# Optimization experiments

Hardware: AMD Instinct MI355X
Metric: run time of the kernel (lower is better)

## Reference

```python
import jax, jax.numpy as jnp
import numpy as np

B, T, C, H = 4, 1024, 1024, 16
HS = C // H  # head_size = 64
EPS = 1e-5


def layer_norm(x, w, b):
    mu = jnp.mean(x, axis=-1, keepdims=True)
    var = jnp.mean(jnp.square(x - mu), axis=-1, keepdims=True)
    return (x - mu) * jax.lax.rsqrt(var + EPS) * w + b


def setup_inputs() -> dict:
    key = jax.random.key(0)
    ks = jax.random.split(key, 12)
    s = 0.02
    return {
        "x": jax.random.normal(ks[0], (B, T, C), jnp.float32),
        "ln1_w": jnp.ones((C,), jnp.float32),
        "ln1_b": jnp.zeros((C,), jnp.float32),
        "Wk": jax.random.normal(ks[1], (H, C, HS), jnp.float32) * s,
        "Wq": jax.random.normal(ks[2], (H, C, HS), jnp.float32) * s,
        "Wv": jax.random.normal(ks[3], (H, C, HS), jnp.float32) * s,
        "Wo": jax.random.normal(ks[4], (C, C), jnp.float32) * s,
        "bo": jnp.zeros((C,), jnp.float32),
        "ln2_w": jnp.ones((C,), jnp.float32),
        "ln2_b": jnp.zeros((C,), jnp.float32),
        "W1": jax.random.normal(ks[5], (C, 4 * C), jnp.float32) * s,
        "b1": jnp.zeros((4 * C,), jnp.float32),
        "prelu_a": jnp.asarray(0.25, jnp.float32),
        "W2": jax.random.normal(ks[6], (4 * C, C), jnp.float32) * s,
        "b2": jnp.zeros((C,), jnp.float32),
    }


def reference(x, ln1_w, ln1_b, Wk, Wq, Wv, Wo, bo, ln2_w, ln2_b, W1, b1, prelu_a, W2, b2):
    # --- self-attention branch (pre-LN) ---
    h = layer_norm(x, ln1_w, ln1_b)  # [B,T,C]
    k = jnp.einsum('btc,hcd->bhtd', h, Wk)
    q = jnp.einsum('btc,hcd->bhtd', h, Wq)
    v = jnp.einsum('btc,hcd->bhtd', h, Wv)
    # NOTE: source computes k @ q^T (not q @ k^T) scaled by n_embd**-0.5
    wei = jnp.einsum('bhtd,bhsd->bhts', k, q) * (C ** -0.5)  # [B,H,T,T]
    causal = jnp.tril(jnp.ones((T, T), bool))
    wei = jnp.where(causal, wei, -jnp.inf)
    wei = jax.nn.softmax(wei, axis=-1)
    out = jnp.einsum('bhts,bhsd->bthd', wei, v).reshape(B, T, C)
    out = out @ Wo + bo
    x = x + out
    # --- feed-forward branch (pre-LN) ---
    h2 = layer_norm(x, ln2_w, ln2_b)
    f = h2 @ W1 + b1
    f = jnp.where(f > 0, f, prelu_a * f)  # PReLU, single scalar param
    f = f @ W2 + b2
    return x + f
```

## Files before the change

### kernel.cpp

```cpp
#include <hip/hip_runtime.h>


typedef __bf16 bf16_t;
typedef __attribute__((ext_vector_type(8))) __bf16 bfx8;
typedef __attribute__((ext_vector_type(4))) __bf16 bfx4;
typedef __attribute__((ext_vector_type(4))) float f32x4;
typedef __attribute__((ext_vector_type(8))) unsigned short u16x8;
typedef unsigned int u32;

#define MFMA_BF16(a, b, c) __builtin_amdgcn_mfma_f32_16x16x32_bf16((a), (b), (c), 0, 0, 0)
#define GLOAD_LDS16(g, l)                                                     \
  __builtin_amdgcn_global_load_lds((__attribute__((address_space(1))) void*)(g), \
                                   (__attribute__((address_space(3))) void*)(l), 16, 0, 0)

__global__ __launch_bounds__(256) void ln_kernel(const float* __restrict__ x,
                                                 const float* __restrict__ w,
                                                 const float* __restrict__ b,
                                                 bf16_t* __restrict__ out) {
  const int row = blockIdx.x;
  const int tid = threadIdx.x;
  const float4 v = reinterpret_cast<const float4*>(x + (size_t)row * 1024)[tid];
  float s = v.x + v.y + v.z + v.w;
  float s2 = v.x * v.x + v.y * v.y + v.z * v.z + v.w * v.w;
#pragma unroll
  for (int off = 1; off < 64; off <<= 1) {
    s += __shfl_xor(s, off);
    s2 += __shfl_xor(s2, off);
  }
  __shared__ float red[8];
  const int wv = tid >> 6;
  if ((tid & 63) == 0) {
    red[wv] = s;
    red[4 + wv] = s2;
  }
  __syncthreads();
  s = red[0] + red[1] + red[2] + red[3];
  s2 = red[4] + red[5] + red[6] + red[7];
  const float mu = s * (1.0f / 1024.0f);
  const float rs = rsqrtf(s2 * (1.0f / 1024.0f) - mu * mu + 1e-5f);
  const float4 wv4 = reinterpret_cast<const float4*>(w)[tid];
  const float4 bv4 = reinterpret_cast<const float4*>(b)[tid];
  bfx4 o;
  o[0] = (bf16_t)((v.x - mu) * rs * wv4.x + bv4.x);
  o[1] = (bf16_t)((v.y - mu) * rs * wv4.y + bv4.y);
  o[2] = (bf16_t)((v.z - mu) * rs * wv4.z + bv4.z);
  o[3] = (bf16_t)((v.w - mu) * rs * wv4.w + bv4.w);
  reinterpret_cast<bfx4*>(out + (size_t)row * 1024)[tid] = o;
}

__device__ __forceinline__ void tc_body(const float* __restrict__ in,
                                        bf16_t* __restrict__ out, int K, int N, int k0,
                                        int n0, float (*tile)[65], int t) {
  const int rl = t >> 4, cl = (t & 15) * 4;
#pragma unroll
  for (int p = 0; p < 4; ++p) {
    const int r = p * 16 + rl;
    const float4 v = *reinterpret_cast<const float4*>(in + (size_t)(k0 + r) * N + n0 + cl);
    tile[r][cl] = v.x;
    tile[r][cl + 1] = v.y;
    tile[r][cl + 2] = v.z;
    tile[r][cl + 3] = v.w;
  }
  __syncthreads();
#pragma unroll
  for (int p = 0; p < 2; ++p) {
    const int idx = p * 256 + t;
    const int n = idx >> 3, kc = (idx & 7) * 8;
    bfx8 o;
#pragma unroll
    for (int i = 0; i < 8; ++i) o[i] = (bf16_t)tile[kc + i][n];
    *reinterpret_cast<bfx8*>(out + (size_t)(n0 + n) * K + k0 + kc) = o;
  }
}

__global__ __launch_bounds__(256) void transpose_cast(const float* __restrict__ in,
                                                      bf16_t* __restrict__ out, int K,
                                                      int N) {
  __shared__ float tile[64][65];
  tc_body(in, out, K, N, blockIdx.x * 64, blockIdx.y * 64, tile, threadIdx.x);
}

__global__ __launch_bounds__(256) void transpose_qkv(const float* __restrict__ Wq,
                                                     const float* __restrict__ Wk,
                                                     const float* __restrict__ Wv,
                                                     bf16_t* __restrict__ out) {
  __shared__ float tile[64][65];
  const int z = blockIdx.y;
  const int sel = z >> 4, h = z & 15;
  const float* in = ((sel == 0) ? Wq : (sel == 1) ? Wk : Wv) + h * 65536;
  bf16_t* o = out + (size_t)sel * 1048576 + h * 65536;
  tc_body(in, o, 1024, 64, blockIdx.x * 64, 0, tile, threadIdx.x);
}

enum { EPI_QKV = 0, EPI_WO = 1, EPI_MLP1 = 2, EPI_FINAL = 3 };

template <int MF>
__device__ __forceinline__ void stage_tile(const bf16_t* __restrict__ A,
                                           const bf16_t* __restrict__ BT, int K, int row0,
                                           int col0, int k0, bf16_t* sA, bf16_t* sB,
                                           int tid) {
#pragma unroll
  for (int j = 0; j < MF; ++j) {
    const int chunk = j * 256 + tid;
    const int r = chunk >> 3, c = chunk & 7;
    const int cs = c ^ (r & 7);
    GLOAD_LDS16(A + (size_t)(row0 + r) * K + k0 + cs * 8, sA + chunk * 8);
  }
#pragma unroll
  for (int j = 0; j < 4; ++j) {
    const int chunk = j * 256 + tid;
    const int r = chunk >> 3, c = chunk & 7;
    const int cs = c ^ (r & 7);
    GLOAD_LDS16(BT + (size_t)(col0 + r) * K + k0 + cs * 8, sB + chunk * 8);
  }
}

template <int EPI, int BM>
__global__ __launch_bounds__(256) void gemm_bt(
    const bf16_t* __restrict__ A, const bf16_t* __restrict__ BT,
    const float* __restrict__ bias, const float* __restrict__ res,
    const float* __restrict__ prelu, float* __restrict__ outf,
    bf16_t* __restrict__ ob0, bf16_t* __restrict__ ob1, bf16_t* __restrict__ ob2,
    int K, int N) {
  constexpr int MF = BM / 32;
  __shared__ __align__(16) bf16_t sA[2][BM * 64];
  __shared__ __align__(16) bf16_t sB[2][128 * 64];
  const int tid = threadIdx.x;
  const int lane = tid & 63;
  const int w = tid >> 6;
  const int wr = w >> 1, wc = w & 1;
  const int row0 = blockIdx.x * BM, col0 = blockIdx.y * 128;

  f32x4 acc[MF][4] = {};

  stage_tile<MF>(A, BT, K, row0, col0, 0, sA[0], sB[0], tid);
  __syncthreads();

  const int nk = K >> 6;
  for (int t = 0; t < nk; ++t) {
    const int cur = t & 1;
    if (t + 1 < nk)
      stage_tile<MF>(A, BT, K, row0, col0, (t + 1) * 64, sA[cur ^ 1], sB[cur ^ 1], tid);
    const bf16_t* __restrict__ pA = sA[cur];
    const bf16_t* __restrict__ pB = sB[cur];
#pragma unroll
    for (int kk = 0; kk < 2; ++kk) {
      bfx8 af[MF], bfr[4];
#pragma unroll
      for (int m = 0; m < MF; ++m) {
        const int r = wr * (BM / 2) + m * 16 + (lane & 15);
        const int c = (kk * 4 + (lane >> 4)) ^ (r & 7);
        af[m] = *reinterpret_cast<const bfx8*>(pA + r * 64 + c * 8);
      }
#pragma unroll
      for (int n = 0; n < 4; ++n) {
        const int r = wc * 64 + n * 16 + (lane & 15);
        const int c = (kk * 4 + (lane >> 4)) ^ (r & 7);
        bfr[n] = *reinterpret_cast<const bfx8*>(pB + r * 64 + c * 8);
      }
#pragma unroll
      for (int m = 0; m < MF; ++m)
#pragma unroll
        for (int n = 0; n < 4; ++n) acc[m][n] = MFMA_BF16(af[m], bfr[n], acc[m][n]);
    }
    __syncthreads();
  }

  const float pa = (EPI == EPI_MLP1) ? prelu[0] : 0.0f;
#pragma unroll
  for (int m = 0; m < MF; ++m) {
#pragma unroll
    for (int n = 0; n < 4; ++n) {
#pragma unroll
      for (int j = 0; j < 4; ++j) {
        const int row = row0 + wr * (BM / 2) + m * 16 + ((lane >> 4) << 2) + j;
        const int col = col0 + wc * 64 + n * 16 + (lane & 15);
        const float v = acc[m][n][j];
        if (EPI == EPI_QKV) {
          const int sel = col >> 10;
          const int h = (col >> 6) & 15, d = col & 63;
          const int bb = row >> 10, t = row & 1023;
          bf16_t* dst = (sel == 0) ? ob0 : (sel == 1) ? ob1 : ob2;
          dst[((size_t)(bb * 16 + h) * 1024 + t) * 64 + d] = (bf16_t)v;
        } else if (EPI == EPI_MLP1) {
          float t = v + bias[col];
          t = (t > 0.0f) ? t : pa * t;
          ob0[(size_t)row * N + col] = (bf16_t)t;
        } else {
          outf[(size_t)row * N + col] = v + bias[col] + res[(size_t)row * N + col];
        }
      }
    }
  }
}

__global__ __launch_bounds__(256) void attn_kernel(const bf16_t* __restrict__ kproj,
                                                   const bf16_t* __restrict__ qproj,
                                                   const bf16_t* __restrict__ vproj,
                                                   bf16_t* __restrict__ att) {
  __shared__ __align__(16) bf16_t sK[2][64 * 64];
  __shared__ __align__(16) bf16_t sVt[2][64 * 64];
  __shared__ __align__(16) bf16_t sP[4][16 * 64];
  const int tid = threadIdx.x, lane = tid & 63, w = tid >> 6;
  const int g = lane >> 4, l15 = lane & 15;
  const int bh = blockIdx.y;
  const size_t head = (size_t)bh * (1024 * 64);
  const int b = bh >> 4, h = bh & 15;
  const int vrow = 2 * (tid >> 3);
  const int vdb = tid & 7;

  for (int half = 0; half < 2; ++half) {
    const int tb = half ? (15 - (int)blockIdx.x) : (int)blockIdx.x;
    const int t0 = tb * 64;
    const int nsb = tb + 1;

    __syncthreads();

    bfx8 aq0, aq1;
    {
      const bf16_t* qrow = kproj + head + (size_t)(t0 + w * 16 + l15) * 64 + g * 8;
      aq0 = *reinterpret_cast<const bfx8*>(qrow);
      aq1 = *reinterpret_cast<const bfx8*>(qrow + 32);
    }

    {
#pragma unroll
      for (int j = 0; j < 2; ++j) {
        const int chunk = j * 256 + tid;
        const int r = chunk >> 3, c = chunk & 7;
        const int cs = c ^ (r & 7);
        GLOAD_LDS16(qproj + head + (size_t)r * 64 + cs * 8, sK[0] + chunk * 8);
      }
      const bf16_t* vp = vproj + head + (size_t)vrow * 64 + vdb * 8;
      const u16x8 v0 = *reinterpret_cast<const u16x8*>(vp);
      const u16x8 v1 = *reinterpret_cast<const u16x8*>(vp + 64);
#pragma unroll
      for (int i = 0; i < 8; ++i) {
        const int d = vdb * 8 + i;
        const int cc = ((vrow >> 3) ^ i ^ vdb) & 7;
        const u32 pk = ((u32)v1[i] << 16) | (u32)v0[i];
        *reinterpret_cast<u32*>(sVt[0] + d * 64 + cc * 8 + (vrow & 7)) = pk;
      }
    }
    __syncthreads();

    f32x4 accO[4] = {};
    float mrun[4], lrun[4];
#pragma unroll
    for (int j = 0; j < 4; ++j) {
      mrun[j] = -1e30f;
      lrun[j] = 0.0f;
    }

    for (int sb = 0; sb < nsb; ++sb) {
      const int cur = sb & 1;
      const bool pf = (sb + 1 < nsb);
      u16x8 v0n, v1n;
      if (pf) {
        const int s0n = (sb + 1) * 64;
#pragma unroll
        for (int j = 0; j < 2; ++j) {
          const int chunk = j * 256 + tid;
          const int r = chunk >> 3, c = chunk & 7;
          const int cs = c ^ (r & 7);
          GLOAD_LDS16(qproj + head + (size_t)(s0n + r) * 64 + cs * 8, sK[cur ^ 1] + chunk * 8);
        }
        const bf16_t* vp = vproj + head + (size_t)(s0n + vrow) * 64 + vdb * 8;
        v0n = *reinterpret_cast<const u16x8*>(vp);
        v1n = *reinterpret_cast<const u16x8*>(vp + 64);
      }

      f32x4 accS[4] = {};
      const bf16_t* sKc = sK[cur];
#pragma unroll
      for (int kk = 0; kk < 2; ++kk) {
        const bfx8 aq = kk ? aq1 : aq0;
#pragma unroll
        for (int n = 0; n < 4; ++n) {
          const int r = n * 16 + l15;
          const int c = (kk * 4 + g) ^ (r & 7);
          const bfx8 bk = *reinterpret_cast<const bfx8*>(sKc + r * 64 + c * 8);
          accS[n] = MFMA_BF16(aq, bk, accS[n]);
        }
      }

      const int rbase = t0 + w * 16 + (g << 2);
      const int cbase = sb * 64 + l15;
#pragma unroll
      for (int j = 0; j < 4; ++j) {
        const int t = rbase + j;
        float mx = -1e30f;
#pragma unroll
        for (int n = 0; n < 4; ++n) {
          float v = accS[n][j] * 0.03125f;
          v = ((cbase + n * 16) <= t) ? v : -1e30f;
          accS[n][j] = v;
          mx = fmaxf(mx, v);
        }
        mx = fmaxf(mx, __shfl_xor(mx, 1));
        mx = fmaxf(mx, __shfl_xor(mx, 2));
        mx = fmaxf(mx, __shfl_xor(mx, 4));
        mx = fmaxf(mx, __shfl_xor(mx, 8));
        const float mnew = fmaxf(mrun[j], mx);
        const float al = __expf(mrun[j] - mnew);
        float rsum = 0.0f;
#pragma unroll
        for (int n = 0; n < 4; ++n) {
          const float p = __expf(accS[n][j] - mnew);
          accS[n][j] = p;
          rsum += p;
        }
        rsum += __shfl_xor(rsum, 1);
        rsum += __shfl_xor(rsum, 2);
        rsum += __shfl_xor(rsum, 4);
        rsum += __shfl_xor(rsum, 8);
        lrun[j] = lrun[j] * al + rsum;
        mrun[j] = mnew;
#pragma unroll
        for (int n = 0; n < 4; ++n) accO[n][j] *= al;
      }

      bf16_t* sPw = sP[w];
#pragma unroll
      for (int n = 0; n < 4; ++n)
#pragma unroll
        for (int j = 0; j < 4; ++j) {
          const int r = (g << 2) + j;
          const int s = n * 16 + l15;
          const int cc = (s >> 3) ^ (r & 7);
          sPw[r * 64 + cc * 8 + (s & 7)] = (bf16_t)accS[n][j];
        }

      const bf16_t* sVc = sVt[cur];
#pragma unroll
      for (int kk = 0; kk < 2; ++kk) {
        bfx8 ap;
        {
          const int r = l15;
          const int c = (kk * 4 + g) ^ (r & 7);
          ap = *reinterpret_cast<const bfx8*>(sPw + r * 64 + c * 8);
        }
#pragma unroll
        for (int n = 0; n < 4; ++n) {
          const int d = n * 16 + l15;
          const int c = (kk * 4 + g) ^ (d & 7) ^ ((d >> 3) & 7);
          const bfx8 bv = *reinterpret_cast<const bfx8*>(sVc + d * 64 + c * 8);
          accO[n] = MFMA_BF16(ap, bv, accO[n]);
        }
      }

      if (pf) {
#pragma unroll
        for (int i = 0; i < 8; ++i) {
          const int d = vdb * 8 + i;
          const int cc = ((vrow >> 3) ^ i ^ vdb) & 7;
          const u32 pk = ((u32)v1n[i] << 16) | (u32)v0n[i];
          *reinterpret_cast<u32*>(sVt[cur ^ 1] + d * 64 + cc * 8 + (vrow & 7)) = pk;
        }
      }
      __syncthreads();
    }

#pragma unroll
    for (int j = 0; j < 4; ++j) {
      const float inv = 1.0f / lrun[j];
      const int t = t0 + w * 16 + (g << 2) + j;
#pragma unroll
      for (int n = 0; n < 4; ++n) {
        const int d = n * 16 + l15;
        att[((size_t)(b * 1024 + t)) * 1024 + h * 64 + d] = (bf16_t)(accO[n][j] * inv);
      }
    }
  }
}

extern "C" void kernel_launch(void* const* d_in, const int* in_sizes, int n_in,
                              void* d_out, int out_size, void* d_ws, size_t ws_size,
                              hipStream_t stream) {
  (void)in_sizes; (void)n_in; (void)out_size; (void)ws_size;
  const float* x = (const float*)d_in[0];
  const float* ln1w = (const float*)d_in[1];
  const float* ln1b = (const float*)d_in[2];
  const float* Wk = (const float*)d_in[3];
  const float* Wq = (const float*)d_in[4];
  const float* Wv = (const float*)d_in[5];
  const float* Wo = (const float*)d_in[6];
  const float* bo = (const float*)d_in[7];
  const float* ln2w = (const float*)d_in[8];
  const float* ln2b = (const float*)d_in[9];
  const float* W1 = (const float*)d_in[10];
  const float* b1 = (const float*)d_in[11];
  const float* pa = (const float*)d_in[12];
  const float* W2 = (const float*)d_in[13];
  const float* b2 = (const float*)d_in[14];
  float* out = (float*)d_out;
  char* ws = (char*)d_ws;
  const size_t MB = 1ull << 20;
  bf16_t* h1 = (bf16_t*)(ws + 0 * MB);
  bf16_t* h2 = (bf16_t*)(ws + 8 * MB);
  bf16_t* qb = (bf16_t*)(ws + 16 * MB);
  bf16_t* kb = (bf16_t*)(ws + 24 * MB);
  bf16_t* vb = (bf16_t*)(ws + 32 * MB);
  bf16_t* attb = (bf16_t*)(ws + 40 * MB);
  bf16_t* fbuf = (bf16_t*)(ws + 48 * MB);
  bf16_t* WqkvT = (bf16_t*)(ws + 80 * MB);
  bf16_t* WoT = (bf16_t*)(ws + 86 * MB);
  bf16_t* W1T = (bf16_t*)(ws + 88 * MB);
  bf16_t* W2T = (bf16_t*)(ws + 96 * MB);

  transpose_qkv<<<dim3(16, 48), 256, 0, stream>>>(Wq, Wk, Wv, WqkvT);
  transpose_cast<<<dim3(16, 16), 256, 0, stream>>>(Wo, WoT, 1024, 1024);
  transpose_cast<<<dim3(16, 64), 256, 0, stream>>>(W1, W1T, 1024, 4096);
  transpose_cast<<<dim3(64, 16), 256, 0, stream>>>(W2, W2T, 4096, 1024);

  ln_kernel<<<4096, 256, 0, stream>>>(x, ln1w, ln1b, h1);
  gemm_bt<EPI_QKV, 128><<<dim3(32, 24), 256, 0, stream>>>(h1, WqkvT, nullptr, nullptr,
                                                          nullptr, nullptr, qb, kb, vb,
                                                          1024, 3072);
  attn_kernel<<<dim3(8, 64), 256, 0, stream>>>(kb, qb, vb, attb);
  gemm_bt<EPI_WO, 64><<<dim3(64, 8), 256, 0, stream>>>(attb, WoT, bo, x, nullptr, out,
                                                       nullptr, nullptr, nullptr, 1024, 1024);
  ln_kernel<<<4096, 256, 0, stream>>>(out, ln2w, ln2b, h2);
  gemm_bt<EPI_MLP1, 128><<<dim3(32, 32), 256, 0, stream>>>(h2, W1T, b1, nullptr, pa, nullptr,
                                                           fbuf, nullptr, nullptr, 1024, 4096);
  gemm_bt<EPI_FINAL, 64><<<dim3(64, 8), 256, 0, stream>>>(fbuf, W2T, b2, out, nullptr, out,
                                                          nullptr, nullptr, nullptr, 4096, 1024);
}
```

Measured before the change: 227.1 us.

## Load GEMM A operand directly to registers and triple-buffer B tiles in LDS

Restructures the bf16 GEMM so each wave loads its A rows straight from global memory into registers (double-buffered) instead of staging them through shared memory. Only B is staged into LDS, now triple-buffered with a prefetch distance of two, and explicit vmcnt waits plus raw barriers replace the full __syncthreads. The Wo and final-projection GEMMs move from 64-row to 128-row tiles, which halves their grid. The aim is to cut LDS traffic and synchronisation stalls and to overlap loads with MFMA work. The cost is higher register pressure, uncoalesced-ish A loads, fewer blocks for the N=1024 GEMMs, and fragile hand-counted vmcnt values.

```diff
diff --git a/kernel.cpp b/kernel.cpp
--- a/kernel.cpp
+++ b/kernel.cpp
@@ -94,87 +94,110 @@
 
 enum { EPI_QKV = 0, EPI_WO = 1, EPI_MLP1 = 2, EPI_FINAL = 3 };
 
-template <int MF>
-__device__ __forceinline__ void stage_tile(const bf16_t* __restrict__ A,
-                                           const bf16_t* __restrict__ BT, int K, int row0,
-                                           int col0, int k0, bf16_t* sA, bf16_t* sB,
-                                           int tid) {
-#pragma unroll
-  for (int j = 0; j < MF; ++j) {
-    const int chunk = j * 256 + tid;
-    const int r = chunk >> 3, c = chunk & 7;
-    const int cs = c ^ (r & 7);
-    GLOAD_LDS16(A + (size_t)(row0 + r) * K + k0 + cs * 8, sA + chunk * 8);
-  }
+__device__ __forceinline__ void load_a(const bf16_t* __restrict__ A, int K, int rowbase,
+                                       int k0, int l15, int g, bfx8 (&ar)[8]) {
+#pragma unroll
+  for (int m = 0; m < 4; ++m)
+#pragma unroll
+    for (int kk = 0; kk < 2; ++kk)
+      ar[m * 2 + kk] = *reinterpret_cast<const bfx8*>(
+          A + (size_t)(rowbase + m * 16 + l15) * K + k0 + kk * 32 + g * 8);
+}
+
+__device__ __forceinline__ void stage_b(const bf16_t* __restrict__ BT, int K, int col0,
+                                        int k0, bf16_t* sBb, int tid) {
 #pragma unroll
   for (int j = 0; j < 4; ++j) {
     const int chunk = j * 256 + tid;
     const int r = chunk >> 3, c = chunk & 7;
     const int cs = c ^ (r & 7);
-    GLOAD_LDS16(BT + (size_t)(col0 + r) * K + k0 + cs * 8, sB + chunk * 8);
-  }
-}
-
-template <int EPI, int BM>
+    GLOAD_LDS16(BT + (size_t)(col0 + r) * K + k0 + cs * 8, sBb + chunk * 8);
+  }
+}
+
+__device__ __forceinline__ void compute_step(const bf16_t* __restrict__ sBc,
+                                             const bfx8 (&ar)[8], f32x4 (&acc)[4][4],
+                                             int wc, int l15, int g) {
+#pragma unroll
+  for (int kk = 0; kk < 2; ++kk) {
+    bfx8 bfr[4];
+#pragma unroll
+    for (int n = 0; n < 4; ++n) {
+      const int r = wc * 64 + n * 16 + l15;
+      const int c = (kk * 4 + g) ^ (r & 7);
+      bfr[n] = *reinterpret_cast<const bfx8*>(sBc + r * 64 + c * 8);
+    }
+#pragma unroll
+    for (int m = 0; m < 4; ++m)
+#pragma unroll
+      for (int n = 0; n < 4; ++n)
+        acc[m][n] = MFMA_BF16(ar[m * 2 + kk], bfr[n], acc[m][n]);
+  }
+}
+
+template <int EPI>
 __global__ __launch_bounds__(256) void gemm_bt(
     const bf16_t* __restrict__ A, const bf16_t* __restrict__ BT,
     const float* __restrict__ bias, const float* __restrict__ res,
     const float* __restrict__ prelu, float* __restrict__ outf,
     bf16_t* __restrict__ ob0, bf16_t* __restrict__ ob1, bf16_t* __restrict__ ob2,
     int K, int N) {
-  constexpr int MF = BM / 32;
-  __shared__ __align__(16) bf16_t sA[2][BM * 64];
-  __shared__ __align__(16) bf16_t sB[2][128 * 64];
+  __shared__ __align__(16) bf16_t sB[3][128 * 64];
   const int tid = threadIdx.x;
   const int lane = tid & 63;
   const int w = tid >> 6;
   const int wr = w >> 1, wc = w & 1;
-  const int row0 = blockIdx.x * BM, col0 = blockIdx.y * 128;
-
-  f32x4 acc[MF][4] = {};
-
-  stage_tile<MF>(A, BT, K, row0, col0, 0, sA[0], sB[0], tid);
-  __syncthreads();
-
+  const int g = lane >> 4, l15 = lane & 15;
+  const int row0 = blockIdx.x * 128, col0 = blockIdx.y * 128;
+  const int rowbase = row0 + wr * 64;
+
+  f32x4 acc[4][4] = {};
+  bfx8 a0[8], a1[8];
   const int nk = K >> 6;
-  for (int t = 0; t < nk; ++t) {
-    const int cur = t & 1;
-    if (t + 1 < nk)
-      stage_tile<MF>(A, BT, K, row0, col0, (t + 1) * 64, sA[cur ^ 1], sB[cur ^ 1], tid);
-    const bf16_t* __restrict__ pA = sA[cur];
-    const bf16_t* __restrict__ pB = sB[cur];
-#pragma unroll
-    for (int kk = 0; kk < 2; ++kk) {
-      bfx8 af[MF], bfr[4];
-#pragma unroll
-      for (int m = 0; m < MF; ++m) {
-        const int r = wr * (BM / 2) + m * 16 + (lane & 15);
-        const int c = (kk * 4 + (lane >> 4)) ^ (r & 7);
-        af[m] = *reinterpret_cast<const bfx8*>(pA + r * 64 + c * 8);
-      }
-#pragma unroll
-      for (int n = 0; n < 4; ++n) {
-        const int r = wc * 64 + n * 16 + (lane & 15);
-        const int c = (kk * 4 + (lane >> 4)) ^ (r & 7);
-        bfr[n] = *reinterpret_cast<const bfx8*>(pB + r * 64 + c * 8);
-      }
-#pragma unroll
-      for (int m = 0; m < MF; ++m)
-#pragma unroll
-        for (int n = 0; n < 4; ++n) acc[m][n] = MFMA_BF16(af[m], bfr[n], acc[m][n]);
-    }
-    __syncthreads();
+
+  load_a(A, K, rowbase, 0, l15, g, a0);
+  stage_b(BT, K, col0, 0, sB[0], tid);
+  stage_b(BT, K, col0, 64, sB[1], tid);
+
+  __builtin_amdgcn_sched_barrier(0);
+  asm volatile("s_waitcnt vmcnt(4)");
+  __builtin_amdgcn_s_barrier();
+  __builtin_amdgcn_sched_barrier(0);
+  load_a(A, K, rowbase, 64, l15, g, a1);
+  stage_b(BT, K, col0, 128, sB[2], tid);
+  compute_step(sB[0], a0, acc, wc, l15, g);
+
+  int cur = 1;
+  for (int t = 1; t < nk; ++t) {
+    __builtin_amdgcn_sched_barrier(0);
+    if (t == nk - 1)
+      asm volatile("s_waitcnt vmcnt(8)");
+    else
+      asm volatile("s_waitcnt vmcnt(12)");
+    __builtin_amdgcn_s_barrier();
+    __builtin_amdgcn_sched_barrier(0);
+    const int prv = (cur == 0) ? 2 : cur - 1;
+    if (t & 1) {
+      if (t + 1 < nk) load_a(A, K, rowbase, (t + 1) * 64, l15, g, a0);
+      if (t + 2 < nk) stage_b(BT, K, col0, (t + 2) * 64, sB[prv], tid);
+      compute_step(sB[cur], a1, acc, wc, l15, g);
+    } else {
+      if (t + 1 < nk) load_a(A, K, rowbase, (t + 1) * 64, l15, g, a1);
+      if (t + 2 < nk) stage_b(BT, K, col0, (t + 2) * 64, sB[prv], tid);
+      compute_step(sB[cur], a0, acc, wc, l15, g);
+    }
+    cur = (cur == 2) ? 0 : cur + 1;
   }
 
   const float pa = (EPI == EPI_MLP1) ? prelu[0] : 0.0f;
 #pragma unroll
-  for (int m = 0; m < MF; ++m) {
+  for (int m = 0; m < 4; ++m) {
 #pragma unroll
     for (int n = 0; n < 4; ++n) {
 #pragma unroll
       for (int j = 0; j < 4; ++j) {
-        const int row = row0 + wr * (BM / 2) + m * 16 + ((lane >> 4) << 2) + j;
-        const int col = col0 + wc * 64 + n * 16 + (lane & 15);
+        const int row = rowbase + m * 16 + (g << 2) + j;
+        const int col = col0 + wc * 64 + n * 16 + l15;
         const float v = acc[m][n][j];
         if (EPI == EPI_QKV) {
           const int sel = col >> 10;
@@ -414,15 +437,14 @@
   transpose_cast<<<dim3(64, 16), 256, 0, stream>>>(W2, W2T, 4096, 1024);
 
   ln_kernel<<<4096, 256, 0, stream>>>(x, ln1w, ln1b, h1);
-  gemm_bt<EPI_QKV, 128><<<dim3(32, 24), 256, 0, stream>>>(h1, WqkvT, nullptr, nullptr,
-                                                          nullptr, nullptr, qb, kb, vb,
-                                                          1024, 3072);
+  gemm_bt<EPI_QKV><<<dim3(32, 24), 256, 0, stream>>>(h1, WqkvT, nullptr, nullptr, nullptr,
+                                                     nullptr, qb, kb, vb, 1024, 3072);
   attn_kernel<<<dim3(8, 64), 256, 0, stream>>>(kb, qb, vb, attb);
-  gemm_bt<EPI_WO, 64><<<dim3(64, 8), 256, 0, stream>>>(attb, WoT, bo, x, nullptr, out,
-                                                       nullptr, nullptr, nullptr, 1024, 1024);
+  gemm_bt<EPI_WO><<<dim3(32, 8), 256, 0, stream>>>(attb, WoT, bo, x, nullptr, out, nullptr,
+                                                   nullptr, nullptr, 1024, 1024);
   ln_kernel<<<4096, 256, 0, stream>>>(out, ln2w, ln2b, h2);
-  gemm_bt<EPI_MLP1, 128><<<dim3(32, 32), 256, 0, stream>>>(h2, W1T, b1, nullptr, pa, nullptr,
-                                                           fbuf, nullptr, nullptr, 1024, 4096);
-  gemm_bt<EPI_FINAL, 64><<<dim3(64, 8), 256, 0, stream>>>(fbuf, W2T, b2, out, nullptr, out,
-                                                          nullptr, nullptr, nullptr, 4096, 1024);
-}
+  gemm_bt<EPI_MLP1><<<dim3(32, 32), 256, 0, stream>>>(h2, W1T, b1, nullptr, pa, nullptr,
+                                                      fbuf, nullptr, nullptr, 1024, 4096);
+  gemm_bt<EPI_FINAL><<<dim3(32, 8), 256, 0, stream>>>(fbuf, W2T, b2, out, nullptr, out,
+                                                      nullptr, nullptr, nullptr, 4096, 1024);
+}
```

Measured after the change: 364.0 us. +60.3%, slower.

## Generalize GEMM tiling with larger tiles and counted vmcnt pipelining

Applied to the files above, without the earlier changes.

Parameterizes the bf16 GEMM over block tile sizes and thread counts, moving the QKV and MLP1 GEMMs to 256x256 tiles with 512 threads and the Wo/W2 GEMMs to 128x128 tiles. The main loop replaces full __syncthreads with a counted s_waitcnt vmcnt so the next tile's async global-to-LDS loads stay in flight while the current tile computes. The larger tiles raise operand reuse per LDS byte but cut the block count (e.g. 192 or 256 blocks), which risks leaving CUs idle and raising register and LDS pressure.

```diff
diff --git a/kernel.cpp b/kernel.cpp
--- a/kernel.cpp
+++ b/kernel.cpp
@@ -94,87 +94,99 @@
 
 enum { EPI_QKV = 0, EPI_WO = 1, EPI_MLP1 = 2, EPI_FINAL = 3 };
 
-template <int MF>
-__device__ __forceinline__ void stage_tile(const bf16_t* __restrict__ A,
-                                           const bf16_t* __restrict__ BT, int K, int row0,
-                                           int col0, int k0, bf16_t* sA, bf16_t* sB,
-                                           int tid) {
-#pragma unroll
-  for (int j = 0; j < MF; ++j) {
-    const int chunk = j * 256 + tid;
-    const int r = chunk >> 3, c = chunk & 7;
-    const int cs = c ^ (r & 7);
-    GLOAD_LDS16(A + (size_t)(row0 + r) * K + k0 + cs * 8, sA + chunk * 8);
-  }
-#pragma unroll
-  for (int j = 0; j < 4; ++j) {
-    const int chunk = j * 256 + tid;
-    const int r = chunk >> 3, c = chunk & 7;
-    const int cs = c ^ (r & 7);
-    GLOAD_LDS16(BT + (size_t)(col0 + r) * K + k0 + cs * 8, sB + chunk * 8);
-  }
-}
-
-template <int EPI, int BM>
-__global__ __launch_bounds__(256) void gemm_bt(
+template <int EPI, int BM, int BN, int NT>
+__global__ __launch_bounds__(NT, 2) void gemm_bt(
     const bf16_t* __restrict__ A, const bf16_t* __restrict__ BT,
     const float* __restrict__ bias, const float* __restrict__ res,
     const float* __restrict__ prelu, float* __restrict__ outf,
     bf16_t* __restrict__ ob0, bf16_t* __restrict__ ob1, bf16_t* __restrict__ ob2,
     int K, int N) {
-  constexpr int MF = BM / 32;
+  constexpr int WM = 2;
+  constexpr int WN = NT / 64 / WM;
+  constexpr int MF = BM / WM / 16;
+  constexpr int NF = BN / WN / 16;
+  constexpr int ACH = BM * 64 / (NT * 8);
+  constexpr int BCH = BN * 64 / (NT * 8);
+  static_assert(ACH + BCH == 8, "counted vmcnt assumes 8 loads per stage");
   __shared__ __align__(16) bf16_t sA[2][BM * 64];
-  __shared__ __align__(16) bf16_t sB[2][128 * 64];
+  __shared__ __align__(16) bf16_t sB[2][BN * 64];
   const int tid = threadIdx.x;
   const int lane = tid & 63;
   const int w = tid >> 6;
-  const int wr = w >> 1, wc = w & 1;
-  const int row0 = blockIdx.x * BM, col0 = blockIdx.y * 128;
-
-  f32x4 acc[MF][4] = {};
-
-  stage_tile<MF>(A, BT, K, row0, col0, 0, sA[0], sB[0], tid);
-  __syncthreads();
-
+  const int wr = w / WN, wc = w % WN;
+  const int g = lane >> 4, l15 = lane & 15;
+  const int row0 = blockIdx.x * BM, col0 = blockIdx.y * BN;
+  const int rowbase = row0 + wr * (BM / WM);
+  const int colbase = wc * (BN / WN);
+
+  f32x4 acc[MF][NF] = {};
+
+  auto stage = [&](int k0, int buf) {
+#pragma unroll
+    for (int j = 0; j < ACH; ++j) {
+      const int chunk = j * NT + tid;
+      const int r = chunk >> 3, c = chunk & 7;
+      GLOAD_LDS16(A + (size_t)(row0 + r) * K + k0 + ((c ^ (r & 7)) * 8),
+                  sA[buf] + chunk * 8);
+    }
+#pragma unroll
+    for (int j = 0; j < BCH; ++j) {
+      const int chunk = j * NT + tid;
+      const int r = chunk >> 3, c = chunk & 7;
+      GLOAD_LDS16(BT + (size_t)(col0 + r) * K + k0 + ((c ^ (r & 7)) * 8),
+                  sB[buf] + chunk * 8);
+    }
+  };
+
+  stage(0, 0);
   const int nk = K >> 6;
   for (int t = 0; t < nk; ++t) {
     const int cur = t & 1;
-    if (t + 1 < nk)
-      stage_tile<MF>(A, BT, K, row0, col0, (t + 1) * 64, sA[cur ^ 1], sB[cur ^ 1], tid);
+    if (t + 1 < nk) {
+      stage((t + 1) << 6, cur ^ 1);
+      __builtin_amdgcn_sched_barrier(0);
+      asm volatile("s_waitcnt vmcnt(8)");
+    } else {
+      __builtin_amdgcn_sched_barrier(0);
+      asm volatile("s_waitcnt vmcnt(0)");
+    }
+    __builtin_amdgcn_s_barrier();
+    __builtin_amdgcn_sched_barrier(0);
     const bf16_t* __restrict__ pA = sA[cur];
     const bf16_t* __restrict__ pB = sB[cur];
 #pragma unroll
     for (int kk = 0; kk < 2; ++kk) {
-      bfx8 af[MF], bfr[4];
+      bfx8 af[MF], bfr[NF];
 #pragma unroll
       for (int m = 0; m < MF; ++m) {
-        const int r = wr * (BM / 2) + m * 16 + (lane & 15);
-        const int c = (kk * 4 + (lane >> 4)) ^ (r & 7);
+        const int r = wr * (BM / WM) + m * 16 + l15;
+        const int c = (kk * 4 + g) ^ (r & 7);
         af[m] = *reinterpret_cast<const bfx8*>(pA + r * 64 + c * 8);
       }
 #pragma unroll
-      for (int n = 0; n < 4; ++n) {
-        const int r = wc * 64 + n * 16 + (lane & 15);
-        const int c = (kk * 4 + (lane >> 4)) ^ (r & 7);
+      for (int n = 0; n < NF; ++n) {
+        const int r = colbase + n * 16 + l15;
+        const int c = (kk * 4 + g) ^ (r & 7);
         bfr[n] = *reinterpret_cast<const bfx8*>(pB + r * 64 + c * 8);
       }
 #pragma unroll
       for (int m = 0; m < MF; ++m)
 #pragma unroll
-        for (int n = 0; n < 4; ++n) acc[m][n] = MFMA_BF16(af[m], bfr[n], acc[m][n]);
-    }
-    __syncthreads();
+        for (int n = 0; n < NF; ++n) acc[m][n] = MFMA_BF16(af[m], bfr[n], acc[m][n]);
+    }
+    __builtin_amdgcn_sched_barrier(0);
+    __builtin_amdgcn_s_barrier();
   }
 
   const float pa = (EPI == EPI_MLP1) ? prelu[0] : 0.0f;
 #pragma unroll
   for (int m = 0; m < MF; ++m) {
 #pragma unroll
-    for (int n = 0; n < 4; ++n) {
+    for (int n = 0; n < NF; ++n) {
 #pragma unroll
       for (int j = 0; j < 4; ++j) {
-        const int row = row0 + wr * (BM / 2) + m * 16 + ((lane >> 4) << 2) + j;
-        const int col = col0 + wc * 64 + n * 16 + (lane & 15);
+        const int row = rowbase + m * 16 + (g << 2) + j;
+        const int col = col0 + colbase + n * 16 + l15;
         const float v = acc[m][n][j];
         if (EPI == EPI_QKV) {
           const int sel = col >> 10;
@@ -414,15 +426,14 @@
   transpose_cast<<<dim3(64, 16), 256, 0, stream>>>(W2, W2T, 4096, 1024);
 
   ln_kernel<<<4096, 256, 0, stream>>>(x, ln1w, ln1b, h1);
-  gemm_bt<EPI_QKV, 128><<<dim3(32, 24), 256, 0, stream>>>(h1, WqkvT, nullptr, nullptr,
-                                                          nullptr, nullptr, qb, kb, vb,
-                                                          1024, 3072);
+  gemm_bt<EPI_QKV, 256, 256, 512><<<dim3(16, 12), 512, 0, stream>>>(
+      h1, WqkvT, nullptr, nullptr, nullptr, nullptr, qb, kb, vb, 1024, 3072);
   attn_kernel<<<dim3(8, 64), 256, 0, stream>>>(kb, qb, vb, attb);
-  gemm_bt<EPI_WO, 64><<<dim3(64, 8), 256, 0, stream>>>(attb, WoT, bo, x, nullptr, out,
-                                                       nullptr, nullptr, nullptr, 1024, 1024);
+  gemm_bt<EPI_WO, 128, 128, 256><<<dim3(32, 8), 256, 0, stream>>>(
+      attb, WoT, bo, x, nullptr, out, nullptr, nullptr, nullptr, 1024, 1024);
   ln_kernel<<<4096, 256, 0, stream>>>(out, ln2w, ln2b, h2);
-  gemm_bt<EPI_MLP1, 128><<<dim3(32, 32), 256, 0, stream>>>(h2, W1T, b1, nullptr, pa, nullptr,
-                                                           fbuf, nullptr, nullptr, 1024, 4096);
-  gemm_bt<EPI_FINAL, 64><<<dim3(64, 8), 256, 0, stream>>>(fbuf, W2T, b2, out, nullptr, out,
-                                                          nullptr, nullptr, nullptr, 4096, 1024);
-}
+  gemm_bt<EPI_MLP1, 256, 256, 512><<<dim3(16, 16), 512, 0, stream>>>(
+      h2, W1T, b1, nullptr, pa, nullptr, fbuf, nullptr, nullptr, 1024, 4096);
+  gemm_bt<EPI_FINAL, 128, 128, 256><<<dim3(32, 8), 256, 0, stream>>>(
+      fbuf, W2T, b2, out, nullptr, out, nullptr, nullptr, nullptr, 4096, 1024);
+}
```

Result: slower. 242.4 us (+6.7%).
